# Kernel optimization log

Hardware: AMD Instinct MI355X
Metric: run time of the kernel (lower is better)

The kernel has to match this reference:

```python
import jax, jax.numpy as jnp
import numpy as np

B, C, D, H, W = 2, 256, 4, 32, 32


def setup_inputs() -> dict:
    key = jax.random.key(0)
    k1, k2, k3, k4, k5 = jax.random.split(key, 5)
    s = 1.0 / np.sqrt(C)
    return {
        "exemplar_features": jax.random.normal(k1, (B, C, D, H, W), jnp.float32),
        "query_features": jax.random.normal(k2, (B, C, D, H, W), jnp.float32),
        "W_ex": jax.random.normal(k3, (C, C), jnp.float32) * s,    # nn.Linear weight (out,in)
        "W_q": jax.random.normal(k4, (C, C), jnp.float32) * s,     # nn.Linear weight (out,in)
        "W_gate": jax.random.normal(k5, (1, C, 1, 1, 1), jnp.float32) * s,  # Conv3d 1x1x1 weight
    }


def reference(exemplar_features, query_features, W_ex, W_q, W_gate):
    b, c, d, h, w = query_features.shape
    n = d * h * w
    ex = exemplar_features.reshape(b, c, n)   # (B,C,N)
    q = query_features.reshape(b, c, n)       # (B,C,N)
    ex_t = jnp.swapaxes(ex, 1, 2)              # (B,N,C)
    q_t = jnp.swapaxes(q, 1, 2)                # (B,N,C)
    # nn.Linear(no bias): x @ W.T
    ex_corr = jnp.einsum('bnc,dc->bnd', ex_t, W_ex)   # (B,N,C)
    q_corr = jnp.einsum('bnc,dc->bnd', q_t, W_q)      # (B,N,C)
    corr_e2q = jnp.einsum('bnc,bcm->bnm', ex_corr, q)  # (B,N,N)
    corr_q2e = jnp.einsum('bnc,bcm->bnm', q_corr, ex)  # (B,N,N)
    # softmax(transpose(corr,1,2), dim=1)
    A_e2q = jax.nn.softmax(jnp.swapaxes(corr_e2q, 1, 2), axis=1)  # (B,N,N)
    A_q2e = jax.nn.softmax(jnp.swapaxes(corr_q2e, 1, 2), axis=1)  # (B,N,N)
    ex_att = jnp.einsum('bcn,bnm->bcm', ex, A_e2q).reshape(b, c, d, h, w)
    q_att = jnp.einsum('bcn,bnm->bcm', q, A_q2e).reshape(b, c, d, h, w)
    # 1x1x1 Conv3d (256 -> 1, no bias) is a channel contraction
    g = W_gate[:, :, 0, 0, 0]  # (1,C)
    ex_mask = jax.nn.sigmoid(jnp.einsum('oc,bcdhw->bodhw', g, ex_att))
    q_mask = jax.nn.sigmoid(jnp.einsum('oc,bcdhw->bodhw', g, q_att))
    return ex_mask, q_mask, A_e2q, A_q2e
```

## Files before the change

### kernel.cpp

```cpp
#include <hip/hip_runtime.h>
#include <math.h>

#define BSZ  2
#define CDIM 256
#define NDIM 4096
#define SHIFT 110.0f

typedef _Float16 f16;
typedef f16  f16x8 __attribute__((ext_vector_type(8)));
typedef float f32x4 __attribute__((ext_vector_type(4)));

static const size_t F16N   = (size_t)BSZ * NDIM * CDIM;
static const size_t WS_FB  = 3 * F16N / 2;

__device__ __forceinline__ void gl_lds16(const void* g, void* l) {
    __builtin_amdgcn_global_load_lds(
        (const __attribute__((address_space(1))) void*)g,
        (__attribute__((address_space(3))) void*)l, 16, 0, 0);
}

__global__ __launch_bounds__(256) void corr_kernel(
    const float* __restrict__ ex, const float* __restrict__ q,
    const float* __restrict__ W_ex, const float* __restrict__ W_q,
    f16* __restrict__ Ah_e, f16* __restrict__ Al_e,
    f16* __restrict__ Ah_q, f16* __restrict__ Al_q)
{
    const int z   = blockIdx.z;
    const int sel = z >> 1;
    const int b   = z & 1;
    const float* feat = sel ? q   : ex;
    const float* W    = sel ? W_q : W_ex;
    f16* Ah = sel ? Ah_q : Ah_e;
    f16* Al = sel ? Al_q : Al_e;

    const int m0  = blockIdx.x * 128;
    const int cc0 = blockIdx.y * 128;
    const int t   = threadIdx.x;
    const int tx  = t & 15;
    const int ty  = t >> 4;

    __shared__ float sA[8][128];
    __shared__ float sB[8][128];

    float acc[8][8];
#pragma unroll
    for (int i = 0; i < 8; i++)
#pragma unroll
        for (int j = 0; j < 8; j++) acc[i][j] = 0.f;

    for (int k0 = 0; k0 < CDIM; k0 += 8) {
        {
            int kk = t >> 5, mi = (t & 31) * 4;
            *(float4*)(&sA[kk][mi]) =
                *(const float4*)(feat + ((size_t)(b * CDIM + k0 + kk)) * NDIM + m0 + mi);
        }
        {
            int ccj = t >> 1, kkb = (t & 1) * 4;
            float4 f = *(const float4*)(W + (size_t)(cc0 + ccj) * CDIM + k0 + kkb);
            sB[kkb + 0][ccj] = f.x; sB[kkb + 1][ccj] = f.y;
            sB[kkb + 2][ccj] = f.z; sB[kkb + 3][ccj] = f.w;
        }
        __syncthreads();
#pragma unroll
        for (int kk = 0; kk < 8; kk++) {
            float a[8], bb[8];
            *(float4*)(a)      = *(const float4*)(&sA[kk][ty * 8]);
            *(float4*)(a + 4)  = *(const float4*)(&sA[kk][ty * 8 + 4]);
            *(float4*)(bb)     = *(const float4*)(&sB[kk][tx * 8]);
            *(float4*)(bb + 4) = *(const float4*)(&sB[kk][tx * 8 + 4]);
#pragma unroll
            for (int i = 0; i < 8; i++)
#pragma unroll
                for (int j = 0; j < 8; j++)
                    acc[i][j] = fmaf(a[i], bb[j], acc[i][j]);
        }
        __syncthreads();
    }
#pragma unroll
    for (int i = 0; i < 8; i++) {
        const int m = m0 + ty * 8 + i;
        f16x8 hv, lv;
#pragma unroll
        for (int j = 0; j < 8; j++) {
            float x = acc[i][j];
            f16 hh = (f16)x;
            hv[j] = hh;
            lv[j] = (f16)(x - (float)hh);
        }
        const size_t off = ((size_t)(b * NDIM + m)) * CDIM + cc0 + tx * 8;
        *(f16x8*)(Ah + off) = hv;
        *(f16x8*)(Al + off) = lv;
    }
}

__global__ __launch_bounds__(256) void pack_b_kernel(
    const float* __restrict__ ex, const float* __restrict__ q,
    f16* __restrict__ Bq, f16* __restrict__ Bex)
{
    const int z   = blockIdx.z;
    const int sel = z >> 1;
    const int b   = z & 1;
    const float* feat = sel ? ex : q;
    f16* outp         = sel ? Bex : Bq;

    const int n0 = blockIdx.x * 64, c0 = blockIdx.y * 64;
    __shared__ float sT[64][65];
    const int t = threadIdx.x;
    const int tn = t & 63, tr = t >> 6;
#pragma unroll
    for (int r = 0; r < 16; ++r) {
        int c = tr + r * 4;
        sT[c][tn] = feat[((size_t)(b * CDIM + c0 + c)) * NDIM + n0 + tn];
    }
    __syncthreads();
#pragma unroll
    for (int r = 0; r < 16; ++r) {
        int n = tr + r * 4;
        outp[((size_t)(b * NDIM + n0 + n)) * CDIM + c0 + tn] = (f16)sT[tn][n];
    }
}

__global__ __launch_bounds__(256) void v_kernel(
    const float* __restrict__ ex, const float* __restrict__ q,
    const float* __restrict__ g,
    float* __restrict__ v_ex, float* __restrict__ v_q)
{
    __shared__ float sg[CDIM];
    const int t = threadIdx.x;
    sg[t] = g[t];
    __syncthreads();

    const int sel = blockIdx.z;
    const int b   = blockIdx.y;
    const float* feat = sel ? q : ex;
    float* outp       = sel ? v_q : v_ex;

    const int n = blockIdx.x * 256 + t;
    float acc = 0.f;
    for (int c = 0; c < CDIM; c++)
        acc = fmaf(sg[c], feat[((size_t)(b * CDIM + c)) * NDIM + n], acc);
    outp[b * NDIM + n] = acc;
}

__global__ __launch_bounds__(256) void score_mfma_kernel(
    const f16* __restrict__ Ah, const f16* __restrict__ Al,
    const f16* __restrict__ Bp, const float* __restrict__ v,
    float* __restrict__ outU,
    float* __restrict__ rowsum, float* __restrict__ rowdot)
{
    const int bb = blockIdx.z;
    const int m0 = blockIdx.x * 128;
    const int n0 = blockIdx.y * 128;
    const int t    = threadIdx.x;
    const int lane = t & 63;
    const int wv   = t >> 6;
    const int lq   = lane >> 4;
    const int ll   = lane & 15;

    __shared__ f16 sAh[8][128][8];
    __shared__ f16 sAl[8][128][8];
    __shared__ f16 sB [8][128][8];

    f32x4 acc[2][8];
#pragma unroll
    for (int mf = 0; mf < 2; mf++)
#pragma unroll
        for (int nf = 0; nf < 8; nf++) acc[mf][nf] = (f32x4)0.f;

    for (int k0 = 0; k0 < CDIM; k0 += 64) {
        if (k0) __syncthreads();
#pragma unroll
        for (int it = 0; it < 4; ++it) {
            const int cidx = (wv * 4 + it) * 64 + lane;
            const int kb = cidx >> 7;
            const int rr = cidx & 127;
            const size_t gA = ((size_t)(bb * NDIM + m0 + rr)) * CDIM + k0 + kb * 8;
            const size_t gB = ((size_t)(bb * NDIM + n0 + rr)) * CDIM + k0 + kb * 8;
            gl_lds16(Ah + gA, (char*)sAh + (size_t)cidx * 16);
            gl_lds16(Al + gA, (char*)sAl + (size_t)cidx * 16);
            gl_lds16(Bp + gB, (char*)sB  + (size_t)cidx * 16);
        }
        __syncthreads();
#pragma unroll
        for (int s = 0; s < 2; ++s) {
            f16x8 bfr[8];
#pragma unroll
            for (int nf = 0; nf < 8; ++nf)
                bfr[nf] = *(const f16x8*)&sB[4 * s + lq][nf * 16 + ll][0];
#pragma unroll
            for (int mf = 0; mf < 2; ++mf) {
                f16x8 ah = *(const f16x8*)&sAh[4 * s + lq][wv * 32 + mf * 16 + ll][0];
                f16x8 al = *(const f16x8*)&sAl[4 * s + lq][wv * 32 + mf * 16 + ll][0];
#pragma unroll
                for (int nf = 0; nf < 8; ++nf) {
                    acc[mf][nf] = __builtin_amdgcn_mfma_f32_16x16x32_f16(ah, bfr[nf], acc[mf][nf], 0, 0, 0);
                    acc[mf][nf] = __builtin_amdgcn_mfma_f32_16x16x32_f16(al, bfr[nf], acc[mf][nf], 0, 0, 0);
                }
            }
        }
    }

    float vv[8];
#pragma unroll
    for (int nf = 0; nf < 8; ++nf) vv[nf] = v[bb * NDIM + n0 + nf * 16 + ll];

    float rs[2][4], rd[2][4];
#pragma unroll
    for (int mf = 0; mf < 2; mf++)
#pragma unroll
        for (int r = 0; r < 4; r++) { rs[mf][r] = 0.f; rd[mf][r] = 0.f; }

#pragma unroll
    for (int mf = 0; mf < 2; ++mf) {
        const int mbase = m0 + wv * 32 + mf * 16 + lq * 4;
#pragma unroll
        for (int nf = 0; nf < 8; ++nf) {
            const int n = n0 + nf * 16 + ll;
            float4 u;
            u.x = __expf(acc[mf][nf][0] - SHIFT);
            u.y = __expf(acc[mf][nf][1] - SHIFT);
            u.z = __expf(acc[mf][nf][2] - SHIFT);
            u.w = __expf(acc[mf][nf][3] - SHIFT);
            *(float4*)(outU + ((size_t)(bb * NDIM + n)) * NDIM + mbase) = u;
            rs[mf][0] += u.x; rs[mf][1] += u.y; rs[mf][2] += u.z; rs[mf][3] += u.w;
            rd[mf][0] += u.x * vv[nf]; rd[mf][1] += u.y * vv[nf];
            rd[mf][2] += u.z * vv[nf]; rd[mf][3] += u.w * vv[nf];
        }
    }
#pragma unroll
    for (int mf = 0; mf < 2; ++mf) {
#pragma unroll
        for (int r = 0; r < 4; ++r) {
#pragma unroll
            for (int off = 1; off < 16; off <<= 1) {
                rs[mf][r] += __shfl_xor(rs[mf][r], off);
                rd[mf][r] += __shfl_xor(rd[mf][r], off);
            }
        }
        if (ll == 0) {
            const int mbase = m0 + wv * 32 + mf * 16 + lq * 4;
#pragma unroll
            for (int r = 0; r < 4; ++r) {
                atomicAdd(rowsum + bb * NDIM + mbase + r, rs[mf][r]);
                atomicAdd(rowdot + bb * NDIM + mbase + r, rd[mf][r]);
            }
        }
    }
}

__global__ __launch_bounds__(256) void mask_kernel(
    const float* __restrict__ sum_e, const float* __restrict__ dot_e,
    const float* __restrict__ sum_q, const float* __restrict__ dot_q,
    float* __restrict__ inv_e, float* __restrict__ inv_q,
    float* __restrict__ outp)
{
    const int idx = blockIdx.x * 256 + threadIdx.x;
    const int j = idx >> 13, i = idx & 8191;
    const float* s = j ? sum_q : sum_e;
    const float* d = j ? dot_q : dot_e;
    float* inv     = j ? inv_q : inv_e;
    const float sv = s[i];
    const float iv = 1.0f / sv;
    inv[i] = iv;
    const float x = d[i] * iv;
    outp[idx] = 1.0f / (1.0f + __expf(-x));
}

__global__ __launch_bounds__(256) void rescale_kernel(
    float* __restrict__ A, const float* __restrict__ inv)
{
    const size_t total4 = (size_t)BSZ * NDIM * NDIM / 4;
    const size_t stride = (size_t)gridDim.x * 256;
    for (size_t i4 = (size_t)blockIdx.x * 256 + threadIdx.x; i4 < total4; i4 += stride) {
        const size_t f = i4 * 4;
        const int m = (int)(f & (NDIM - 1));
        const int b = (int)(f >> 24);
        float4 u  = *(float4*)(A + f);
        float4 iv = *(const float4*)(inv + b * NDIM + m);
        u.x *= iv.x; u.y *= iv.y; u.z *= iv.z; u.w *= iv.w;
        *(float4*)(A + f) = u;
    }
}

extern "C" void kernel_launch(void* const* d_in, const int* in_sizes, int n_in,
                              void* d_out, int out_size, void* d_ws, size_t ws_size,
                              hipStream_t stream)
{
    const float* ex   = (const float*)d_in[0];
    const float* q    = (const float*)d_in[1];
    const float* W_ex = (const float*)d_in[2];
    const float* W_q  = (const float*)d_in[3];
    const float* g    = (const float*)d_in[4];
    float* outp = (float*)d_out;

    float* A_e2q = outp + 16384;
    float* A_q2e = A_e2q + (size_t)BSZ * NDIM * NDIM;

    f16* Ah_e = (f16*)A_q2e;
    f16* Al_e = Ah_e + F16N;
    f16* Bq   = Al_e + F16N;

    f16* Ah_q = (f16*)d_ws;
    f16* Al_q = Ah_q + F16N;
    f16* Bex  = Al_q + F16N;
    float* wsf  = (float*)d_ws + WS_FB;
    float* v_ex = wsf;
    float* v_q  = wsf + 8192;
    float* sum_e = wsf + 2 * 8192;
    float* dot_e = wsf + 3 * 8192;
    float* sum_q = wsf + 4 * 8192;
    float* dot_q = wsf + 5 * 8192;
    float* inv_e = wsf + 6 * 8192;
    float* inv_q = wsf + 7 * 8192;

    hipMemsetAsync(sum_e, 0, 4 * 8192 * sizeof(float), stream);

    corr_kernel<<<dim3(NDIM / 128, CDIM / 128, 2 * BSZ), 256, 0, stream>>>(
        ex, q, W_ex, W_q, Ah_e, Al_e, Ah_q, Al_q);

    pack_b_kernel<<<dim3(NDIM / 64, CDIM / 64, 2 * BSZ), 256, 0, stream>>>(
        ex, q, Bq, Bex);

    v_kernel<<<dim3(NDIM / 256, BSZ, 2), 256, 0, stream>>>(ex, q, g, v_ex, v_q);

    score_mfma_kernel<<<dim3(32, 32, BSZ), 256, 0, stream>>>(
        Ah_e, Al_e, Bq, v_ex, A_e2q, sum_e, dot_e);
    score_mfma_kernel<<<dim3(32, 32, BSZ), 256, 0, stream>>>(
        Ah_q, Al_q, Bex, v_q, A_q2e, sum_q, dot_q);

    mask_kernel<<<64, 256, 0, stream>>>(sum_e, dot_e, sum_q, dot_q, inv_e, inv_q, outp);

    rescale_kernel<<<32768, 256, 0, stream>>>(A_e2q, inv_e);
    rescale_kernel<<<32768, 256, 0, stream>>>(A_q2e, inv_q);
}
```

Before: 562.6 us.

## Fuse softmax normalization into score kernel via ticketed row-group spin barrier

The score kernel now takes a ticket from an atomic counter to set its tile order, and keeps the exponentiated scores in registers instead of writing them out. It then waits on a per-row-group counter until all 32 tiles of that row group have added their row sums, and writes the already normalized values. This removes the separate rescale pass, which read and wrote the full 2x4096x4096 attention matrix twice. The cost is blocks spinning while they wait, and the scheme relies on ticket ordering so that tiles being waited on are already resident and cannot deadlock.

After: 1.073 ms. +90.7%, slower.

```diff
diff --git a/kernel.cpp b/kernel.cpp
--- a/kernel.cpp
+++ b/kernel.cpp
@@ -146,20 +146,30 @@
     const f16* __restrict__ Ah, const f16* __restrict__ Al,
     const f16* __restrict__ Bp, const float* __restrict__ v,
     float* __restrict__ outU,
-    float* __restrict__ rowsum, float* __restrict__ rowdot)
-{
-    const int bb = blockIdx.z;
-    const int m0 = blockIdx.x * 128;
-    const int n0 = blockIdx.y * 128;
+    float* __restrict__ rowsum, float* __restrict__ rowdot,
+    int* __restrict__ ticket, int* __restrict__ done)
+{
     const int t    = threadIdx.x;
     const int lane = t & 63;
     const int wv   = t >> 6;
     const int lq   = lane >> 4;
     const int ll   = lane & 15;
 
+    __shared__ int s_tk;
+    if (t == 0)
+        s_tk = __hip_atomic_fetch_add(ticket, 1, __ATOMIC_RELAXED,
+                                      __HIP_MEMORY_SCOPE_AGENT);
+
     __shared__ f16 sAh[8][128][8];
     __shared__ f16 sAl[8][128][8];
     __shared__ f16 sB [8][128][8];
+
+    __syncthreads();
+    const int tk = s_tk;
+    const int bb = tk >> 10;
+    const int m0 = ((tk >> 5) & 31) << 7;
+    const int n0 = (tk & 31) << 7;
+    int* const drow = done + (tk >> 5);
 
     f32x4 acc[2][8];
 #pragma unroll
@@ -212,16 +222,15 @@
 
 #pragma unroll
     for (int mf = 0; mf < 2; ++mf) {
-        const int mbase = m0 + wv * 32 + mf * 16 + lq * 4;
 #pragma unroll
         for (int nf = 0; nf < 8; ++nf) {
-            const int n = n0 + nf * 16 + ll;
             float4 u;
             u.x = __expf(acc[mf][nf][0] - SHIFT);
             u.y = __expf(acc[mf][nf][1] - SHIFT);
             u.z = __expf(acc[mf][nf][2] - SHIFT);
             u.w = __expf(acc[mf][nf][3] - SHIFT);
-            *(float4*)(outU + ((size_t)(bb * NDIM + n)) * NDIM + mbase) = u;
+            acc[mf][nf][0] = u.x; acc[mf][nf][1] = u.y;
+            acc[mf][nf][2] = u.z; acc[mf][nf][3] = u.w;
             rs[mf][0] += u.x; rs[mf][1] += u.y; rs[mf][2] += u.z; rs[mf][3] += u.w;
             rd[mf][0] += u.x * vv[nf]; rd[mf][1] += u.y * vv[nf];
             rd[mf][2] += u.z * vv[nf]; rd[mf][3] += u.w * vv[nf];
@@ -246,40 +255,51 @@
             }
         }
     }
+
+    __syncthreads();
+    if (t == 0) {
+        __threadfence();
+        __hip_atomic_fetch_add(drow, 1, __ATOMIC_RELEASE,
+                               __HIP_MEMORY_SCOPE_AGENT);
+        while (__hip_atomic_load(drow, __ATOMIC_ACQUIRE,
+                                 __HIP_MEMORY_SCOPE_AGENT) < 32)
+            __builtin_amdgcn_s_sleep(1);
+    }
+    __syncthreads();
+
+#pragma unroll
+    for (int mf = 0; mf < 2; ++mf) {
+        const int mbase = m0 + wv * 32 + mf * 16 + lq * 4;
+        float iv[4];
+#pragma unroll
+        for (int r = 0; r < 4; ++r)
+            iv[r] = 1.0f / __hip_atomic_load(rowsum + bb * NDIM + mbase + r,
+                                             __ATOMIC_RELAXED,
+                                             __HIP_MEMORY_SCOPE_AGENT);
+#pragma unroll
+        for (int nf = 0; nf < 8; ++nf) {
+            const int n = n0 + nf * 16 + ll;
+            float4 u;
+            u.x = acc[mf][nf][0] * iv[0];
+            u.y = acc[mf][nf][1] * iv[1];
+            u.z = acc[mf][nf][2] * iv[2];
+            u.w = acc[mf][nf][3] * iv[3];
+            *(float4*)(outU + ((size_t)(bb * NDIM + n)) * NDIM + mbase) = u;
+        }
+    }
 }
 
 __global__ __launch_bounds__(256) void mask_kernel(
     const float* __restrict__ sum_e, const float* __restrict__ dot_e,
     const float* __restrict__ sum_q, const float* __restrict__ dot_q,
-    float* __restrict__ inv_e, float* __restrict__ inv_q,
     float* __restrict__ outp)
 {
     const int idx = blockIdx.x * 256 + threadIdx.x;
     const int j = idx >> 13, i = idx & 8191;
     const float* s = j ? sum_q : sum_e;
     const float* d = j ? dot_q : dot_e;
-    float* inv     = j ? inv_q : inv_e;
-    const float sv = s[i];
-    const float iv = 1.0f / sv;
-    inv[i] = iv;
-    const float x = d[i] * iv;
+    const float x = d[i] * (1.0f / s[i]);
     outp[idx] = 1.0f / (1.0f + __expf(-x));
-}
-
-__global__ __launch_bounds__(256) void rescale_kernel(
-    float* __restrict__ A, const float* __restrict__ inv)
-{
-    const size_t total4 = (size_t)BSZ * NDIM * NDIM / 4;
-    const size_t stride = (size_t)gridDim.x * 256;
-    for (size_t i4 = (size_t)blockIdx.x * 256 + threadIdx.x; i4 < total4; i4 += stride) {
-        const size_t f = i4 * 4;
-        const int m = (int)(f & (NDIM - 1));
-        const int b = (int)(f >> 24);
-        float4 u  = *(float4*)(A + f);
-        float4 iv = *(const float4*)(inv + b * NDIM + m);
-        u.x *= iv.x; u.y *= iv.y; u.z *= iv.z; u.w *= iv.w;
-        *(float4*)(A + f) = u;
-    }
 }
 
 extern "C" void kernel_launch(void* const* d_in, const int* in_sizes, int n_in,
@@ -310,10 +330,12 @@
     float* dot_e = wsf + 3 * 8192;
     float* sum_q = wsf + 4 * 8192;
     float* dot_q = wsf + 5 * 8192;
-    float* inv_e = wsf + 6 * 8192;
-    float* inv_q = wsf + 7 * 8192;
-
-    hipMemsetAsync(sum_e, 0, 4 * 8192 * sizeof(float), stream);
+    int* done_e = (int*)(wsf + 6 * 8192);
+    int* done_q = done_e + 64;
+    int* tick_e = done_q + 64;
+    int* tick_q = tick_e + 1;
+
+    hipMemsetAsync(sum_e, 0, 4 * 8192 * sizeof(float) + 130 * sizeof(int), stream);
 
     corr_kernel<<<dim3(NDIM / 128, CDIM / 128, 2 * BSZ), 256, 0, stream>>>(
         ex, q, W_ex, W_q, Ah_e, Al_e, Ah_q, Al_q);
@@ -323,13 +345,10 @@
 
     v_kernel<<<dim3(NDIM / 256, BSZ, 2), 256, 0, stream>>>(ex, q, g, v_ex, v_q);
 
-    score_mfma_kernel<<<dim3(32, 32, BSZ), 256, 0, stream>>>(
-        Ah_e, Al_e, Bq, v_ex, A_e2q, sum_e, dot_e);
-    score_mfma_kernel<<<dim3(32, 32, BSZ), 256, 0, stream>>>(
-        Ah_q, Al_q, Bex, v_q, A_q2e, sum_q, dot_q);
-
-    mask_kernel<<<64, 256, 0, stream>>>(sum_e, dot_e, sum_q, dot_q, inv_e, inv_q, outp);
-
-    rescale_kernel<<<32768, 256, 0, stream>>>(A_e2q, inv_e);
-    rescale_kernel<<<32768, 256, 0, stream>>>(A_q2e, inv_q);
-}
+    score_mfma_kernel<<<2048, 256, 0, stream>>>(
+        Ah_e, Al_e, Bq, v_ex, A_e2q, sum_e, dot_e, tick_e, done_e);
+    score_mfma_kernel<<<2048, 256, 0, stream>>>(
+        Ah_q, Al_q, Bex, v_q, A_q2e, sum_q, dot_q, tick_q, done_q);
+
+    mask_kernel<<<64, 256, 0, stream>>>(sum_e, dot_e, sum_q, dot_q, outp);
+}
```

## Recompute score GEMM in a second pass to fuse normalization into attention stores

Applied to the files above, without the earlier changes.

The score GEMM is split into two passes. The first pass computes only the row sums and value dots, using atomics, and stores no scores. A second GEMM pass recomputes the scores, multiplies by the inverse row sums, and writes the normalized attention through an LDS-staged, coalesced transpose. This removes the unnormalized write and the separate full read-modify-write rescale over both 4096x4096 attention matrices, at the cost of doing the MFMA GEMM twice. The GEMM now also loads operands directly from global memory into registers instead of staging them in LDS, and uses launch_bounds occupancy hints.

Measured after the change: 670.7 us. +19.2%, slower.

```diff
diff --git a/kernel.cpp b/kernel.cpp
--- a/kernel.cpp
+++ b/kernel.cpp
@@ -12,12 +12,6 @@
 
 static const size_t F16N   = (size_t)BSZ * NDIM * CDIM;
 static const size_t WS_FB  = 3 * F16N / 2;
-
-__device__ __forceinline__ void gl_lds16(const void* g, void* l) {
-    __builtin_amdgcn_global_load_lds(
-        (const __attribute__((address_space(1))) void*)g,
-        (__attribute__((address_space(3))) void*)l, 16, 0, 0);
-}
 
 __global__ __launch_bounds__(256) void corr_kernel(
     const float* __restrict__ ex, const float* __restrict__ q,
@@ -142,10 +136,36 @@
     outp[b * NDIM + n] = acc;
 }
 
-__global__ __launch_bounds__(256) void score_mfma_kernel(
+__device__ __forceinline__ void score_accumulate(
+    const f16* __restrict__ Ah, const f16* __restrict__ Al,
+    const f16* __restrict__ Bp,
+    int bb, int m0, int n0, int wv, int lq, int ll,
+    f32x4 acc[2][8])
+{
+    const size_t rowB = ((size_t)(bb * NDIM + n0 + ll)) * CDIM + lq * 8;
+    const size_t rowA = ((size_t)(bb * NDIM + m0 + wv * 32 + ll)) * CDIM + lq * 8;
+#pragma unroll 1
+    for (int k0 = 0; k0 < CDIM; k0 += 32) {
+        f16x8 bfr[8];
+#pragma unroll
+        for (int nf = 0; nf < 8; ++nf)
+            bfr[nf] = *(const f16x8*)(Bp + rowB + (size_t)nf * 16 * CDIM + k0);
+#pragma unroll
+        for (int mf = 0; mf < 2; ++mf) {
+            f16x8 ah = *(const f16x8*)(Ah + rowA + (size_t)mf * 16 * CDIM + k0);
+            f16x8 al = *(const f16x8*)(Al + rowA + (size_t)mf * 16 * CDIM + k0);
+#pragma unroll
+            for (int nf = 0; nf < 8; ++nf) {
+                acc[mf][nf] = __builtin_amdgcn_mfma_f32_16x16x32_f16(ah, bfr[nf], acc[mf][nf], 0, 0, 0);
+                acc[mf][nf] = __builtin_amdgcn_mfma_f32_16x16x32_f16(al, bfr[nf], acc[mf][nf], 0, 0, 0);
+            }
+        }
+    }
+}
+
+__global__ __launch_bounds__(256, 4) void sum_score_kernel(
     const f16* __restrict__ Ah, const f16* __restrict__ Al,
     const f16* __restrict__ Bp, const float* __restrict__ v,
-    float* __restrict__ outU,
     float* __restrict__ rowsum, float* __restrict__ rowdot)
 {
     const int bb = blockIdx.z;
@@ -157,48 +177,13 @@
     const int lq   = lane >> 4;
     const int ll   = lane & 15;
 
-    __shared__ f16 sAh[8][128][8];
-    __shared__ f16 sAl[8][128][8];
-    __shared__ f16 sB [8][128][8];
-
     f32x4 acc[2][8];
 #pragma unroll
     for (int mf = 0; mf < 2; mf++)
 #pragma unroll
         for (int nf = 0; nf < 8; nf++) acc[mf][nf] = (f32x4)0.f;
 
-    for (int k0 = 0; k0 < CDIM; k0 += 64) {
-        if (k0) __syncthreads();
-#pragma unroll
-        for (int it = 0; it < 4; ++it) {
-            const int cidx = (wv * 4 + it) * 64 + lane;
-            const int kb = cidx >> 7;
-            const int rr = cidx & 127;
-            const size_t gA = ((size_t)(bb * NDIM + m0 + rr)) * CDIM + k0 + kb * 8;
-            const size_t gB = ((size_t)(bb * NDIM + n0 + rr)) * CDIM + k0 + kb * 8;
-            gl_lds16(Ah + gA, (char*)sAh + (size_t)cidx * 16);
-            gl_lds16(Al + gA, (char*)sAl + (size_t)cidx * 16);
-            gl_lds16(Bp + gB, (char*)sB  + (size_t)cidx * 16);
-        }
-        __syncthreads();
-#pragma unroll
-        for (int s = 0; s < 2; ++s) {
-            f16x8 bfr[8];
-#pragma unroll
-            for (int nf = 0; nf < 8; ++nf)
-                bfr[nf] = *(const f16x8*)&sB[4 * s + lq][nf * 16 + ll][0];
-#pragma unroll
-            for (int mf = 0; mf < 2; ++mf) {
-                f16x8 ah = *(const f16x8*)&sAh[4 * s + lq][wv * 32 + mf * 16 + ll][0];
-                f16x8 al = *(const f16x8*)&sAl[4 * s + lq][wv * 32 + mf * 16 + ll][0];
-#pragma unroll
-                for (int nf = 0; nf < 8; ++nf) {
-                    acc[mf][nf] = __builtin_amdgcn_mfma_f32_16x16x32_f16(ah, bfr[nf], acc[mf][nf], 0, 0, 0);
-                    acc[mf][nf] = __builtin_amdgcn_mfma_f32_16x16x32_f16(al, bfr[nf], acc[mf][nf], 0, 0, 0);
-                }
-            }
-        }
-    }
+    score_accumulate(Ah, Al, Bp, bb, m0, n0, wv, lq, ll, acc);
 
     float vv[8];
 #pragma unroll
@@ -212,19 +197,15 @@
 
 #pragma unroll
     for (int mf = 0; mf < 2; ++mf) {
-        const int mbase = m0 + wv * 32 + mf * 16 + lq * 4;
 #pragma unroll
         for (int nf = 0; nf < 8; ++nf) {
-            const int n = n0 + nf * 16 + ll;
-            float4 u;
-            u.x = __expf(acc[mf][nf][0] - SHIFT);
-            u.y = __expf(acc[mf][nf][1] - SHIFT);
-            u.z = __expf(acc[mf][nf][2] - SHIFT);
-            u.w = __expf(acc[mf][nf][3] - SHIFT);
-            *(float4*)(outU + ((size_t)(bb * NDIM + n)) * NDIM + mbase) = u;
-            rs[mf][0] += u.x; rs[mf][1] += u.y; rs[mf][2] += u.z; rs[mf][3] += u.w;
-            rd[mf][0] += u.x * vv[nf]; rd[mf][1] += u.y * vv[nf];
-            rd[mf][2] += u.z * vv[nf]; rd[mf][3] += u.w * vv[nf];
+            float u0 = __expf(acc[mf][nf][0] - SHIFT);
+            float u1 = __expf(acc[mf][nf][1] - SHIFT);
+            float u2 = __expf(acc[mf][nf][2] - SHIFT);
+            float u3 = __expf(acc[mf][nf][3] - SHIFT);
+            rs[mf][0] += u0; rs[mf][1] += u1; rs[mf][2] += u2; rs[mf][3] += u3;
+            rd[mf][0] += u0 * vv[nf]; rd[mf][1] += u1 * vv[nf];
+            rd[mf][2] += u2 * vv[nf]; rd[mf][3] += u3 * vv[nf];
         }
     }
 #pragma unroll
@@ -244,6 +225,64 @@
                 atomicAdd(rowsum + bb * NDIM + mbase + r, rs[mf][r]);
                 atomicAdd(rowdot + bb * NDIM + mbase + r, rd[mf][r]);
             }
+        }
+    }
+}
+
+__global__ __launch_bounds__(256, 4) void store_score_kernel(
+    const f16* __restrict__ Ah, const f16* __restrict__ Al,
+    const f16* __restrict__ Bp, const float* __restrict__ inv,
+    float* __restrict__ outA)
+{
+    const int bb = blockIdx.z;
+    const int m0 = blockIdx.x * 128;
+    const int n0 = blockIdx.y * 128;
+    const int t    = threadIdx.x;
+    const int lane = t & 63;
+    const int wv   = t >> 6;
+    const int lq   = lane >> 4;
+    const int ll   = lane & 15;
+
+    __shared__ float sOut[64 * 132];
+
+    f32x4 acc[2][8];
+#pragma unroll
+    for (int mf = 0; mf < 2; mf++)
+#pragma unroll
+        for (int nf = 0; nf < 8; nf++) acc[mf][nf] = (f32x4)0.f;
+
+    score_accumulate(Ah, Al, Bp, bb, m0, n0, wv, lq, ll, acc);
+
+    float4 iv[2];
+#pragma unroll
+    for (int mf = 0; mf < 2; ++mf)
+        iv[mf] = *(const float4*)(inv + bb * NDIM + m0 + wv * 32 + mf * 16 + lq * 4);
+
+#pragma unroll
+    for (int round = 0; round < 2; ++round) {
+        if (round) __syncthreads();
+#pragma unroll
+        for (int nfl = 0; nfl < 4; ++nfl) {
+            const int nf = round * 4 + nfl;
+#pragma unroll
+            for (int mf = 0; mf < 2; ++mf) {
+                float4 u;
+                u.x = __expf(acc[mf][nf][0] - SHIFT) * iv[mf].x;
+                u.y = __expf(acc[mf][nf][1] - SHIFT) * iv[mf].y;
+                u.z = __expf(acc[mf][nf][2] - SHIFT) * iv[mf].z;
+                u.w = __expf(acc[mf][nf][3] - SHIFT) * iv[mf].w;
+                *(float4*)(&sOut[(nfl * 16 + ll) * 132 + wv * 32 + mf * 16 + lq * 4]) = u;
+            }
+        }
+        __syncthreads();
+#pragma unroll
+        for (int rep = 0; rep < 8; ++rep) {
+            const int w   = rep * 256 + t;
+            const int row = w >> 5;
+            const int col = (w & 31) * 4;
+            float4 u = *(const float4*)(&sOut[row * 132 + col]);
+            const int n = n0 + round * 64 + row;
+            *(float4*)(outA + ((size_t)(bb * NDIM + n)) * NDIM + m0 + col) = u;
         }
     }
 }
@@ -260,26 +299,10 @@
     const float* d = j ? dot_q : dot_e;
     float* inv     = j ? inv_q : inv_e;
     const float sv = s[i];
-    const float iv = 1.0f / sv;
-    inv[i] = iv;
-    const float x = d[i] * iv;
+    const float ivv = 1.0f / sv;
+    inv[i] = ivv;
+    const float x = d[i] * ivv;
     outp[idx] = 1.0f / (1.0f + __expf(-x));
-}
-
-__global__ __launch_bounds__(256) void rescale_kernel(
-    float* __restrict__ A, const float* __restrict__ inv)
-{
-    const size_t total4 = (size_t)BSZ * NDIM * NDIM / 4;
-    const size_t stride = (size_t)gridDim.x * 256;
-    for (size_t i4 = (size_t)blockIdx.x * 256 + threadIdx.x; i4 < total4; i4 += stride) {
-        const size_t f = i4 * 4;
-        const int m = (int)(f & (NDIM - 1));
-        const int b = (int)(f >> 24);
-        float4 u  = *(float4*)(A + f);
-        float4 iv = *(const float4*)(inv + b * NDIM + m);
-        u.x *= iv.x; u.y *= iv.y; u.z *= iv.z; u.w *= iv.w;
-        *(float4*)(A + f) = u;
-    }
 }
 
 extern "C" void kernel_launch(void* const* d_in, const int* in_sizes, int n_in,
@@ -323,13 +346,16 @@
 
     v_kernel<<<dim3(NDIM / 256, BSZ, 2), 256, 0, stream>>>(ex, q, g, v_ex, v_q);
 
-    score_mfma_kernel<<<dim3(32, 32, BSZ), 256, 0, stream>>>(
-        Ah_e, Al_e, Bq, v_ex, A_e2q, sum_e, dot_e);
-    score_mfma_kernel<<<dim3(32, 32, BSZ), 256, 0, stream>>>(
-        Ah_q, Al_q, Bex, v_q, A_q2e, sum_q, dot_q);
-
-    mask_kernel<<<64, 256, 0, stream>>>(sum_e, dot_e, sum_q, dot_q, inv_e, inv_q, outp);
-
-    rescale_kernel<<<32768, 256, 0, stream>>>(A_e2q, inv_e);
-    rescale_kernel<<<32768, 256, 0, stream>>>(A_q2e, inv_q);
-}
+    sum_score_kernel<<<dim3(32, 32, BSZ), 256, 0, stream>>>(
+        Ah_e, Al_e, Bq, v_ex, sum_e, dot_e);
+    sum_score_kernel<<<dim3(32, 32, BSZ), 256, 0, stream>>>(
+        Ah_q, Al_q, Bex, v_q, sum_q, dot_q);
+
+    mask_kernel<<<64, 256, 0, stream>>>(sum_e, dot_e, sum_q, dot_q,
+                                        inv_e, inv_q, outp);
+
+    store_score_kernel<<<dim3(32, 32, BSZ), 256, 0, stream>>>(
+        Ah_e, Al_e, Bq, inv_e, A_e2q);
+    store_score_kernel<<<dim3(32, 32, BSZ), 256, 0, stream>>>(
+        Ah_q, Al_q, Bex, inv_q, A_q2e);
+}
```

## Double-buffer B tile in LDS and load A fragments directly from global

Applied to the files above, without the earlier changes.

The score MFMA kernel no longer stages the A hi/lo tiles through shared memory. Each wave now reads its own A fragments straight from global memory into registers. The B tile is double-buffered in LDS, so the next k-chunk's async global-to-LDS load overlaps the current chunk's MFMAs, and one barrier per iteration is dropped. The aim is to cut LDS traffic and barrier stalls, at the risk of uncoalesced 16-byte global loads for A that are exposed to latency.

New measurement: 536.5 us. 1.05x faster.

```diff
diff --git a/kernel.cpp b/kernel.cpp
--- a/kernel.cpp
+++ b/kernel.cpp
@@ -157,9 +157,18 @@
     const int lq   = lane >> 4;
     const int ll   = lane & 15;
 
-    __shared__ f16 sAh[8][128][8];
-    __shared__ f16 sAl[8][128][8];
-    __shared__ f16 sB [8][128][8];
+    __shared__ f16 sB[2][8][128][8];
+
+    const size_t srcB = ((size_t)(bb * NDIM + n0 + (t & 127))) * CDIM + (t >> 7) * 8;
+
+#define STAGE_B(buf_, k0_) do {                                              \
+        char* _dst = (char*)(&sB[buf_][0][0][0]) + (size_t)t * 16;           \
+        _Pragma("unroll")                                                    \
+        for (int _it = 0; _it < 4; ++_it)                                    \
+            gl_lds16(Bp + srcB + (k0_) + _it * 16, _dst + _it * 4096);       \
+    } while (0)
+
+    const size_t rowA = ((size_t)(bb * NDIM + m0 + wv * 32 + ll)) * CDIM + lq * 8;
 
     f32x4 acc[2][8];
 #pragma unroll
@@ -167,38 +176,43 @@
 #pragma unroll
         for (int nf = 0; nf < 8; nf++) acc[mf][nf] = (f32x4)0.f;
 
-    for (int k0 = 0; k0 < CDIM; k0 += 64) {
-        if (k0) __syncthreads();
-#pragma unroll
-        for (int it = 0; it < 4; ++it) {
-            const int cidx = (wv * 4 + it) * 64 + lane;
-            const int kb = cidx >> 7;
-            const int rr = cidx & 127;
-            const size_t gA = ((size_t)(bb * NDIM + m0 + rr)) * CDIM + k0 + kb * 8;
-            const size_t gB = ((size_t)(bb * NDIM + n0 + rr)) * CDIM + k0 + kb * 8;
-            gl_lds16(Ah + gA, (char*)sAh + (size_t)cidx * 16);
-            gl_lds16(Al + gA, (char*)sAl + (size_t)cidx * 16);
-            gl_lds16(Bp + gB, (char*)sB  + (size_t)cidx * 16);
-        }
-        __syncthreads();
+    STAGE_B(0, 0);
+    __syncthreads();
+
+#pragma unroll 1
+    for (int kc = 0; kc < 4; ++kc) {
+        const int k0 = kc * 64;
+        const int cb = kc & 1;
+
+        f16x8 afr_h[2][2], afr_l[2][2];
+#pragma unroll
+        for (int s = 0; s < 2; ++s)
+#pragma unroll
+            for (int mf = 0; mf < 2; ++mf) {
+                afr_h[s][mf] = *(const f16x8*)(Ah + rowA + (size_t)mf * 16 * CDIM + k0 + s * 32);
+                afr_l[s][mf] = *(const f16x8*)(Al + rowA + (size_t)mf * 16 * CDIM + k0 + s * 32);
+            }
+
+        if (kc < 3) STAGE_B((kc + 1) & 1, k0 + 64);
+
 #pragma unroll
         for (int s = 0; s < 2; ++s) {
             f16x8 bfr[8];
 #pragma unroll
             for (int nf = 0; nf < 8; ++nf)
-                bfr[nf] = *(const f16x8*)&sB[4 * s + lq][nf * 16 + ll][0];
+                bfr[nf] = *(const f16x8*)&sB[cb][4 * s + lq][nf * 16 + ll][0];
 #pragma unroll
             for (int mf = 0; mf < 2; ++mf) {
-                f16x8 ah = *(const f16x8*)&sAh[4 * s + lq][wv * 32 + mf * 16 + ll][0];
-                f16x8 al = *(const f16x8*)&sAl[4 * s + lq][wv * 32 + mf * 16 + ll][0];
 #pragma unroll
                 for (int nf = 0; nf < 8; ++nf) {
-                    acc[mf][nf] = __builtin_amdgcn_mfma_f32_16x16x32_f16(ah, bfr[nf], acc[mf][nf], 0, 0, 0);
-                    acc[mf][nf] = __builtin_amdgcn_mfma_f32_16x16x32_f16(al, bfr[nf], acc[mf][nf], 0, 0, 0);
+                    acc[mf][nf] = __builtin_amdgcn_mfma_f32_16x16x32_f16(afr_h[s][mf], bfr[nf], acc[mf][nf], 0, 0, 0);
+                    acc[mf][nf] = __builtin_amdgcn_mfma_f32_16x16x32_f16(afr_l[s][mf], bfr[nf], acc[mf][nf], 0, 0, 0);
                 }
             }
         }
-    }
+        if (kc < 3) __syncthreads();
+    }
+#undef STAGE_B
 
     float vv[8];
 #pragma unroll
```
